# Optimization experiments

Measured on AMD Instinct MI355X. Metric: run time of the kernel, lower is better.

Reference implementation:

```python
import jax, jax.numpy as jnp
import numpy as np

EPS = 1e-6  # eps assumed for rms/unit norm (repo uses a small eps; math identical up to eps)

def rms_norm(x):
    # normalize so RMS over last dim == 1
    return x * jax.lax.rsqrt(jnp.mean(x * x, axis=-1, keepdims=True) + EPS)

def unit_norm(w):
    # normalize each output row of the weight to unit L2 norm
    return w * jax.lax.rsqrt(jnp.sum(w * w, axis=-1, keepdims=True) + EPS)

def setup_inputs() -> dict:
    key = jax.random.key(0)
    k1, k2, k3 = jax.random.split(key, 3)
    B, S, D = 4, 2048, 2048
    x = jax.random.normal(k1, (B, S, D), dtype=jnp.float32)
    w_in = jax.random.normal(k2, (3 * D, D), dtype=jnp.float32)
    w_out = jax.random.normal(k3, (D, D), dtype=jnp.float32)
    return {"x": x, "w_in": w_in, "w_out": w_out}

def reference(x, w_in, w_out):
    B, S, D = x.shape
    H = 16
    hd = D // H
    # MPLinear in-projection with unit-normalized weight rows
    qkv = jnp.einsum("bsd,fd->bsf", x, unit_norm(w_in))  # [B,S,3D]
    qkv = qkv.reshape(B, S, 3, H, hd).transpose(2, 0, 3, 1, 4)  # [3,B,H,S,hd]
    q, k, v = qkv[0], qkv[1], qkv[2]
    q = rms_norm(q)
    k = rms_norm(k)
    # scaled dot product attention, causal, default scale 1/sqrt(hd)
    scores = jnp.einsum("bhqd,bhkd->bhqk", q, k) / jnp.sqrt(jnp.float32(hd))
    causal_mask = jnp.tril(jnp.ones((S, S), dtype=bool))
    scores = jnp.where(causal_mask, scores, jnp.finfo(scores.dtype).min)
    attn = jax.nn.softmax(scores, axis=-1)
    a = jnp.einsum("bhqk,bhkd->bhqd", attn, v)  # [B,H,S,hd]
    a = rms_norm(a)
    a = a.transpose(0, 2, 1, 3).reshape(B, S, D)
    return jnp.einsum("bsd,fd->bsf", a, unit_norm(w_out))
```

## Files before the change

kernel.cpp:

```cpp
#include <hip/hip_runtime.h>

typedef float f32x4 __attribute__((ext_vector_type(4)));
typedef __bf16 bf16x8 __attribute__((ext_vector_type(8)));

#define EPSF 1e-6f
#define AS1 __attribute__((address_space(1)))
#define AS3 __attribute__((address_space(3)))

__device__ static inline void gl_lds16(const __bf16* g, __bf16* l) {
  __builtin_amdgcn_global_load_lds((const AS1 void*)g, (AS3 void*)l, 16, 0, 0);
}

__global__ __launch_bounds__(256) void prep(const float* __restrict__ x,
                                            const float* __restrict__ w_in,
                                            const float* __restrict__ w_out,
                                            __bf16* __restrict__ xb,
                                            __bf16* __restrict__ w_in_n,
                                            __bf16* __restrict__ w_out_n) {
  __shared__ float red[4];
  const int bid = blockIdx.x;
  const int t = threadIdx.x;
  if (bid < 8192) {
    const float* src = (bid < 6144) ? (w_in + (size_t)bid * 2048)
                                    : (w_out + (size_t)(bid - 6144) * 2048);
    __bf16* dst = (bid < 6144) ? (w_in_n + (size_t)bid * 2048)
                               : (w_out_n + (size_t)(bid - 6144) * 2048);
    float4 v[2];
    float ss = 0.f;
#pragma unroll
    for (int i = 0; i < 2; i++) {
      v[i] = ((const float4*)src)[t + i * 256];
      ss += v[i].x * v[i].x + v[i].y * v[i].y + v[i].z * v[i].z + v[i].w * v[i].w;
    }
#pragma unroll
    for (int m = 32; m >= 1; m >>= 1) ss += __shfl_xor(ss, m);
    if ((t & 63) == 0) red[t >> 6] = ss;
    __syncthreads();
    float tot = red[0] + red[1] + red[2] + red[3];
    float sc = rsqrtf(tot + EPSF);
#pragma unroll
    for (int i = 0; i < 2; i++) {
      int c0 = (t + i * 256) * 4;
      dst[c0 + 0] = (__bf16)(v[i].x * sc);
      dst[c0 + 1] = (__bf16)(v[i].y * sc);
      dst[c0 + 2] = (__bf16)(v[i].z * sc);
      dst[c0 + 3] = (__bf16)(v[i].w * sc);
    }
  } else {
    size_t i = ((size_t)(bid - 8192) * 256 + t) * 8;
    float4 a = ((const float4*)(x + i))[0];
    float4 b = ((const float4*)(x + i))[1];
    bf16x8 o;
    o[0] = (__bf16)a.x; o[1] = (__bf16)a.y; o[2] = (__bf16)a.z; o[3] = (__bf16)a.w;
    o[4] = (__bf16)b.x; o[5] = (__bf16)b.y; o[6] = (__bf16)b.z; o[7] = (__bf16)b.w;
    *(bf16x8*)(xb + i) = o;
  }
}

#define LDSOFF(r_, blk_) ((r_) * 64 + (((blk_) ^ ((r_) & 7)) * 8))
#define SA(bb_, c_, kt_) gl_lds16(gA + (long)(c_) * 64 * K + (long)(kt_) * 64, &As[bb_][(c_) * 4096 + t * 8])
#define SB(bb_, c_, kt_) gl_lds16(gB + (long)(c_) * 64 * K + (long)(kt_) * 64, &Bs[bb_][(c_) * 4096 + t * 8])

template <int MODE>
__global__ __launch_bounds__(512) void gemm8(const __bf16* __restrict__ A,
                                             const __bf16* __restrict__ W,
                                             float* __restrict__ C,
                                             __bf16* __restrict__ Cb,
                                             __bf16* __restrict__ Vtb,
                                             int M, int N, int K) {
  __shared__ __bf16 As[2][16384];
  __shared__ __bf16 Bs[2][16384];
  __shared__ float rsum[8][128];

  const int gx = gridDim.x;
  const int nwg = gx * gridDim.y;
  int wg = blockIdx.y * gx + blockIdx.x;
  wg = (wg & 7) * (nwg >> 3) + (wg >> 3);
  const int bx = wg % gx, by = wg / gx;

  const int t = threadIdx.x;
  const int lane = t & 63, w = t >> 6;
  const int wr = w >> 2, wc = w & 3;
  const int wrb = wr * 128, wcb = wc * 64;
  const int fr = lane & 15, fq = lane >> 4;
  const long m0 = (long)by * 256;
  const long n0 = (long)bx * 256;
  const int NT = K >> 6;

  const int srow = t >> 3;
  const int sblk = (t & 7) ^ (srow & 7);
  const __bf16* gA = A + (m0 + srow) * (long)K + sblk * 8;
  const __bf16* gB = W + (n0 + srow) * (long)K + sblk * 8;

  f32x4 acc[8][4];
#pragma unroll
  for (int i = 0; i < 8; i++)
#pragma unroll
    for (int j = 0; j < 4; j++)
#pragma unroll
      for (int c = 0; c < 4; c++) acc[i][j][c] = 0.f;

  SA(0, 0, 0); SA(0, 1, 0); SA(0, 2, 0); SA(0, 3, 0);
  SB(0, 0, 0); SB(0, 1, 0); SB(0, 2, 0); SB(0, 3, 0);
  SA(1, 0, 1); SA(1, 2, 1);
  SB(1, 0, 1); SB(1, 1, 1); SB(1, 2, 1); SB(1, 3, 1);
  asm volatile("s_waitcnt vmcnt(6)" ::: "memory");
  __builtin_amdgcn_s_barrier();

  auto tile_step = [&](int kt, int b) {
    bf16x8 a0[4][2], b01[2][2];
#pragma unroll
    for (int i = 0; i < 4; i++)
#pragma unroll
      for (int ks = 0; ks < 2; ks++)
        a0[i][ks] = *(const bf16x8*)&As[b][LDSOFF(wrb + i * 16 + fr, ks * 4 + fq)];
#pragma unroll
    for (int j = 0; j < 2; j++)
#pragma unroll
      for (int ks = 0; ks < 2; ks++)
        b01[j][ks] = *(const bf16x8*)&Bs[b][LDSOFF(wcb + j * 16 + fr, ks * 4 + fq)];
    if (kt + 1 < NT) { SA(b ^ 1, 1, kt + 1); SA(b ^ 1, 3, kt + 1); }
    __builtin_amdgcn_s_setprio(1);
#pragma unroll
    for (int i = 0; i < 4; i++)
#pragma unroll
      for (int j = 0; j < 2; j++)
#pragma unroll
        for (int ks = 0; ks < 2; ks++)
          acc[i][j] = __builtin_amdgcn_mfma_f32_16x16x32_bf16(a0[i][ks], b01[j][ks], acc[i][j], 0, 0, 0);
    __builtin_amdgcn_s_setprio(0);
    __builtin_amdgcn_sched_barrier(0);
    __builtin_amdgcn_s_barrier();

    bf16x8 b23[2][2];
#pragma unroll
    for (int j = 0; j < 2; j++)
#pragma unroll
      for (int ks = 0; ks < 2; ks++)
        b23[j][ks] = *(const bf16x8*)&Bs[b][LDSOFF(wcb + (2 + j) * 16 + fr, ks * 4 + fq)];
    if (kt + 2 < NT) { SA(b, 0, kt + 2); SA(b, 2, kt + 2); }
    __builtin_amdgcn_s_setprio(1);
#pragma unroll
    for (int i = 0; i < 4; i++)
#pragma unroll
      for (int j = 0; j < 2; j++)
#pragma unroll
        for (int ks = 0; ks < 2; ks++)
          acc[i][2 + j] = __builtin_amdgcn_mfma_f32_16x16x32_bf16(a0[i][ks], b23[j][ks], acc[i][2 + j], 0, 0, 0);
    __builtin_amdgcn_s_setprio(0);
    __builtin_amdgcn_sched_barrier(0);
    __builtin_amdgcn_s_barrier();

    bf16x8 a1[4][2];
#pragma unroll
    for (int i = 0; i < 4; i++)
#pragma unroll
      for (int ks = 0; ks < 2; ks++)
        a1[i][ks] = *(const bf16x8*)&As[b][LDSOFF(wrb + 64 + i * 16 + fr, ks * 4 + fq)];
    if (kt + 2 < NT) { SB(b, 0, kt + 2); SB(b, 1, kt + 2); SB(b, 2, kt + 2); SB(b, 3, kt + 2); }
    __builtin_amdgcn_s_setprio(1);
#pragma unroll
    for (int i = 0; i < 4; i++)
#pragma unroll
      for (int j = 0; j < 2; j++)
#pragma unroll
        for (int ks = 0; ks < 2; ks++)
          acc[4 + i][j] = __builtin_amdgcn_mfma_f32_16x16x32_bf16(a1[i][ks], b01[j][ks], acc[4 + i][j], 0, 0, 0);
#pragma unroll
    for (int i = 0; i < 4; i++)
#pragma unroll
      for (int j = 0; j < 2; j++)
#pragma unroll
        for (int ks = 0; ks < 2; ks++)
          acc[4 + i][2 + j] = __builtin_amdgcn_mfma_f32_16x16x32_bf16(a1[i][ks], b23[j][ks], acc[4 + i][2 + j], 0, 0, 0);
    __builtin_amdgcn_s_setprio(0);
    if (kt >= NT - 2)
      asm volatile("s_waitcnt vmcnt(0)" ::: "memory");
    else
      asm volatile("s_waitcnt vmcnt(6)" ::: "memory");
    __builtin_amdgcn_sched_barrier(0);
    __builtin_amdgcn_s_barrier();
  };

  for (int kt = 0; kt < NT; kt += 2) {
    tile_step(kt, 0);
    tile_step(kt + 1, 1);
  }

  if (MODE == 0) {
#pragma unroll
    for (int i = 0; i < 8; i++)
#pragma unroll
      for (int j = 0; j < 4; j++)
#pragma unroll
        for (int r = 0; r < 4; r++) {
          long row = m0 + wrb + i * 16 + fq * 4 + r;
          long col = n0 + wcb + j * 16 + fr;
          C[row * N + col] = acc[i][j][r];
        }
  } else {
    const int tt = (int)(n0 >> 11);
    const int hh = (int)(((n0 >> 7) + (wc >> 1)) & 15);
    const long e0 = (long)(wc & 1) * 64;
    if (tt < 2) {
#pragma unroll
      for (int i = 0; i < 8; i++)
#pragma unroll
        for (int r = 0; r < 4; r++) {
          float s2 = 0.f;
#pragma unroll
          for (int j = 0; j < 4; j++) s2 += acc[i][j][r] * acc[i][j][r];
          s2 += __shfl_xor(s2, 1);
          s2 += __shfl_xor(s2, 2);
          s2 += __shfl_xor(s2, 4);
          s2 += __shfl_xor(s2, 8);
          if (fr == 0) rsum[w][i * 16 + fq * 4 + r] = s2;
        }
      __syncthreads();
#pragma unroll
      for (int i = 0; i < 8; i++)
#pragma unroll
        for (int r = 0; r < 4; r++) {
          int rl = i * 16 + fq * 4 + r;
          float tot = rsum[w][rl] + rsum[w ^ 1][rl];
          float sc = rsqrtf(tot * (1.f / 128.f) + EPSF);
          long row = m0 + wrb + rl;
          long bb = row >> 11, ss = row & 2047;
          __bf16* base = Cb + ((((long)tt * 4 + bb) * 16 + hh) * 2048 + ss) * 128 + e0;
#pragma unroll
          for (int j = 0; j < 4; j++)
            base[j * 16 + fr] = (__bf16)(acc[i][j][r] * sc);
        }
    } else {
#pragma unroll
      for (int i = 0; i < 8; i++)
#pragma unroll
        for (int r = 0; r < 4; r++) {
          long row = m0 + wrb + i * 16 + fq * 4 + r;
          long bb = row >> 11, ss = row & 2047;
#pragma unroll
          for (int j = 0; j < 4; j++)
            Vtb[((bb * 16 + hh) * 128 + e0 + j * 16 + fr) * 2048 + ss] = (__bf16)acc[i][j][r];
        }
    }
  }
}

__global__ __launch_bounds__(256, 3) void attn(const __bf16* __restrict__ qkv,
                                               const __bf16* __restrict__ vt,
                                               __bf16* __restrict__ an) {
  __shared__ __bf16 Ks[64 * 128];
  __shared__ __bf16 Vs[128 * 64];
  __shared__ __bf16 plds[8][16 * 40];
  const int L = blockIdx.x;
  const int qt = L >> 6;
  const int bh = (L & 7) + 8 * ((L >> 3) & 7);
  const int t = threadIdx.x;
  const int lane = t & 63, w = t >> 6;
  const int fr = lane & 15, fq = lane >> 4;
  const int swz = fr & 7;
  const __bf16* Q = qkv + (long)bh * 262144;
  const __bf16* Kbh = qkv + 16777216L + (long)bh * 262144;
  const __bf16* Vbh = vt + (long)bh * 262144;
  const float sc2 = 0.08838834764831845f * 1.4426950408889634f;
  const float MFIX = 20.0f;
  const int b = bh >> 4, h = bh & 15;

  const __bf16* gK = Kbh + (long)(t >> 4) * 128 + ((t & 15) ^ ((t >> 4) & 7)) * 8;
  const __bf16* gV = Vbh + (long)(t >> 3) * 2048 + ((t & 7) ^ ((t >> 3) & 7)) * 8;
  __bf16* lK = &Ks[t * 8];
  __bf16* lV = &Vs[t * 8];

#pragma unroll 1
  for (int side = 0; side < 2; side++) {
    const int qi = side ? (15 - qt) : qt;
    const int q0 = qi * 128 + w * 32;
    const int cha = q0 >> 5;
    bf16x8 qf[2][4];
#pragma unroll
    for (int f = 0; f < 2; f++)
#pragma unroll
      for (int ec = 0; ec < 4; ec++)
        qf[f][ec] = *(const bf16x8*)(Q + (long)(q0 + f * 16 + fr) * 128 + ec * 32 + fq * 8);
    float lacc[2][4];
#pragma unroll
    for (int f = 0; f < 2; f++)
#pragma unroll
      for (int r = 0; r < 4; r++) lacc[f][r] = 0.f;
    f32x4 oacc[2][8];
#pragma unroll
    for (int f = 0; f < 2; f++)
#pragma unroll
      for (int e = 0; e < 8; e++)
#pragma unroll
        for (int c = 0; c < 4; c++) oacc[f][e][c] = 0.f;

    const int nst = 2 * qi + 2;
#pragma unroll 1
    for (int st = 0; st < nst; st++) {
      const long k0 = (long)st * 64;
#pragma unroll
      for (int j = 0; j < 4; j++) gl_lds16(gK + (k0 + j * 16) * 128, lK + j * 2048);
#pragma unroll
      for (int j = 0; j < 4; j++) gl_lds16(gV + (long)j * 32 * 2048 + k0, lV + j * 2048);
      __syncthreads();
#pragma unroll
      for (int half = 0; half < 2; half++) {
        const int k32 = (int)k0 + half * 32;
        const int ch = k32 >> 5;
        if (ch <= cha) {
          f32x4 sa[2][2];
#pragma unroll
          for (int f = 0; f < 2; f++)
#pragma unroll
            for (int ct = 0; ct < 2; ct++)
#pragma unroll
              for (int c = 0; c < 4; c++) sa[f][ct][c] = 0.f;
#pragma unroll
          for (int ct = 0; ct < 2; ct++) {
#pragma unroll
            for (int ec = 0; ec < 4; ec++) {
              bf16x8 kf = *(const bf16x8*)(&Ks[(half * 32 + ct * 16 + fr) * 128 +
                                               ((ec * 4 + fq) ^ swz) * 8]);
              sa[0][ct] = __builtin_amdgcn_mfma_f32_16x16x32_bf16(qf[0][ec], kf, sa[0][ct], 0, 0, 0);
              sa[1][ct] = __builtin_amdgcn_mfma_f32_16x16x32_bf16(qf[1][ec], kf, sa[1][ct], 0, 0, 0);
            }
          }
#pragma unroll
          for (int f = 0; f < 2; f++) {
            __bf16* pwf = plds[(w << 1) + f];
            if (ch == cha) {
#pragma unroll
              for (int r = 0; r < 4; r++) {
                int qg = q0 + f * 16 + fq * 4 + r;
                float p0 = exp2f(((k32 + fr) <= qg) ? sa[f][0][r] * sc2 - MFIX : -1e30f);
                float p1 = exp2f(((k32 + 16 + fr) <= qg) ? sa[f][1][r] * sc2 - MFIX : -1e30f);
                lacc[f][r] += p0 + p1;
                pwf[(fq * 4 + r) * 40 + fr] = (__bf16)p0;
                pwf[(fq * 4 + r) * 40 + 16 + fr] = (__bf16)p1;
              }
            } else {
#pragma unroll
              for (int r = 0; r < 4; r++) {
                float p0 = exp2f(__builtin_fmaf(sa[f][0][r], sc2, -MFIX));
                float p1 = exp2f(__builtin_fmaf(sa[f][1][r], sc2, -MFIX));
                lacc[f][r] += p0 + p1;
                pwf[(fq * 4 + r) * 40 + fr] = (__bf16)p0;
                pwf[(fq * 4 + r) * 40 + 16 + fr] = (__bf16)p1;
              }
            }
          }
          bf16x8 pa0 = *(const bf16x8*)(&plds[(w << 1) + 0][fr * 40 + fq * 8]);
          bf16x8 pa1 = *(const bf16x8*)(&plds[(w << 1) + 1][fr * 40 + fq * 8]);
#pragma unroll
          for (int e = 0; e < 8; e++) {
            bf16x8 vf = *(const bf16x8*)(&Vs[(e * 16 + fr) * 64 +
                                             ((half * 4 + fq) ^ swz) * 8]);
            oacc[0][e] = __builtin_amdgcn_mfma_f32_16x16x32_bf16(pa0, vf, oacc[0][e], 0, 0, 0);
            oacc[1][e] = __builtin_amdgcn_mfma_f32_16x16x32_bf16(pa1, vf, oacc[1][e], 0, 0, 0);
          }
        }
      }
      __syncthreads();
    }
#pragma unroll
    for (int f = 0; f < 2; f++)
#pragma unroll
      for (int r = 0; r < 4; r++) {
        float ls = lacc[f][r];
        ls += __shfl_xor(ls, 1);
        ls += __shfl_xor(ls, 2);
        ls += __shfl_xor(ls, 4);
        ls += __shfl_xor(ls, 8);
        float inv = 1.0f / ls;
        float ssq = 0.f;
#pragma unroll
        for (int e = 0; e < 8; e++) { float v = oacc[f][e][r] * inv; ssq += v * v; }
        ssq += __shfl_xor(ssq, 1);
        ssq += __shfl_xor(ssq, 2);
        ssq += __shfl_xor(ssq, 4);
        ssq += __shfl_xor(ssq, 8);
        float rsc = rsqrtf(ssq * (1.f / 128.f) + EPSF) * inv;
        long s = q0 + f * 16 + fq * 4 + r;
        __bf16* dst = an + ((long)b * 2048 + s) * 2048 + h * 128;
#pragma unroll
        for (int e = 0; e < 8; e++) dst[e * 16 + fr] = (__bf16)(oacc[f][e][r] * rsc);
      }
  }
}

extern "C" void kernel_launch(void* const* d_in, const int* in_sizes, int n_in,
                              void* d_out, int out_size, void* d_ws, size_t ws_size,
                              hipStream_t stream) {
  const float* x = (const float*)d_in[0];
  const float* w_in = (const float*)d_in[1];
  const float* w_out = (const float*)d_in[2];
  float* out = (float*)d_out;
  char* ws = (char*)d_ws;

  __bf16* w_in_n = (__bf16*)(ws);
  __bf16* w_out_n = (__bf16*)(ws + 25165824);
  __bf16* xb = (__bf16*)(ws + 33554432);
  __bf16* an = xb;
  __bf16* qkv = (__bf16*)(ws + 67108864);
  __bf16* vt = (__bf16*)(ws + 167772160);

  prep<<<16384, 256, 0, stream>>>(x, w_in, w_out, xb, w_in_n, w_out_n);
  gemm8<1><<<dim3(24, 32), 512, 0, stream>>>(xb, w_in_n, nullptr, qkv, vt, 8192, 6144, 2048);
  attn<<<512, 256, 0, stream>>>(qkv, vt, an);
  gemm8<0><<<dim3(8, 32), 512, 0, stream>>>(an, w_out_n, out, nullptr, nullptr, 8192, 2048, 2048);
}
```

Measured before the change: 517.9 us.

## Double-buffer K/V tiles in attention with 512-thread blocks and 256-row query tiles

The attention kernel now uses 8 waves per block covering 256 query rows, so each staged K/V tile is shared by twice as many waves. K/V tiles are double-buffered in LDS, with the next tile prefetched via global_load_lds while the current one is consumed, using vmcnt waits and raw barriers. The score-then-PV step is reorganized to process both 32-key halves of a 64-key tile together, with separate diagonal-masking paths. LDS use grows (two K/V buffers plus a larger P scratch), which lowers occupancy and halves the grid to 256 blocks, so CU load balance may suffer.

```diff
diff --git a/kernel.cpp b/kernel.cpp
--- a/kernel.cpp
+++ b/kernel.cpp
@@ -246,15 +246,15 @@
   }
 }
 
-__global__ __launch_bounds__(256, 3) void attn(const __bf16* __restrict__ qkv,
-                                               const __bf16* __restrict__ vt,
-                                               __bf16* __restrict__ an) {
-  __shared__ __bf16 Ks[64 * 128];
-  __shared__ __bf16 Vs[128 * 64];
-  __shared__ __bf16 plds[8][16 * 40];
+__global__ __launch_bounds__(512) void attn(const __bf16* __restrict__ qkv,
+                                            const __bf16* __restrict__ vt,
+                                            __bf16* __restrict__ an) {
+  __shared__ __bf16 Ks[2][64 * 128];
+  __shared__ __bf16 Vs[2][128 * 64];
+  __shared__ __bf16 plds[32][16 * 40];
   const int L = blockIdx.x;
-  const int qt = L >> 6;
-  const int bh = (L & 7) + 8 * ((L >> 3) & 7);
+  const int qp = L >> 6;
+  const int bh = L & 63;
   const int t = threadIdx.x;
   const int lane = t & 63, w = t >> 6;
   const int fr = lane & 15, fq = lane >> 4;
@@ -268,14 +268,24 @@
 
   const __bf16* gK = Kbh + (long)(t >> 4) * 128 + ((t & 15) ^ ((t >> 4) & 7)) * 8;
   const __bf16* gV = Vbh + (long)(t >> 3) * 2048 + ((t & 7) ^ ((t >> 3) & 7)) * 8;
-  __bf16* lK = &Ks[t * 8];
-  __bf16* lV = &Vs[t * 8];
+
+  auto stage = [&](int st, int buf) {
+    const long k0 = (long)st * 64;
+    gl_lds16(gK + k0 * 128, &Ks[buf][t * 8]);
+    gl_lds16(gK + (k0 + 32) * 128, &Ks[buf][4096 + t * 8]);
+    gl_lds16(gV + k0, &Vs[buf][t * 8]);
+    gl_lds16(gV + 64L * 2048 + k0, &Vs[buf][4096 + t * 8]);
+  };
 
 #pragma unroll 1
   for (int side = 0; side < 2; side++) {
-    const int qi = side ? (15 - qt) : qt;
-    const int q0 = qi * 128 + w * 32;
+    const int qi = side ? (7 - qp) : qp;
+    const int q0 = qi * 256 + w * 32;
     const int cha = q0 >> 5;
+    const int nst = 4 * qi + 4;
+
+    stage(0, 0);
+    stage(1, 1);
     bf16x8 qf[2][4];
 #pragma unroll
     for (int f = 0; f < 2; f++)
@@ -295,73 +305,132 @@
 #pragma unroll
         for (int c = 0; c < 4; c++) oacc[f][e][c] = 0.f;
 
-    const int nst = 2 * qi + 2;
 #pragma unroll 1
     for (int st = 0; st < nst; st++) {
-      const long k0 = (long)st * 64;
-#pragma unroll
-      for (int j = 0; j < 4; j++) gl_lds16(gK + (k0 + j * 16) * 128, lK + j * 2048);
-#pragma unroll
-      for (int j = 0; j < 4; j++) gl_lds16(gV + (long)j * 32 * 2048 + k0, lV + j * 2048);
-      __syncthreads();
-#pragma unroll
-      for (int half = 0; half < 2; half++) {
-        const int k32 = (int)k0 + half * 32;
-        const int ch = k32 >> 5;
-        if (ch <= cha) {
-          f32x4 sa[2][2];
+      if (st + 1 < nst)
+        asm volatile("s_waitcnt vmcnt(4)" ::: "memory");
+      else
+        asm volatile("s_waitcnt vmcnt(0)" ::: "memory");
+      __builtin_amdgcn_s_barrier();
+      const __bf16* Kb = Ks[st & 1];
+      const __bf16* Vb = Vs[st & 1];
+      const int k0 = st * 64;
+      const int ch0 = 2 * st, ch1 = 2 * st + 1;
+      if (ch1 <= cha) {
+        f32x4 sa[2][2][2];
+#pragma unroll
+        for (int hh2 = 0; hh2 < 2; hh2++)
 #pragma unroll
           for (int f = 0; f < 2; f++)
 #pragma unroll
             for (int ct = 0; ct < 2; ct++)
 #pragma unroll
-              for (int c = 0; c < 4; c++) sa[f][ct][c] = 0.f;
-#pragma unroll
-          for (int ct = 0; ct < 2; ct++) {
+              for (int c = 0; c < 4; c++) sa[hh2][f][ct][c] = 0.f;
+#pragma unroll
+        for (int hh2 = 0; hh2 < 2; hh2++)
+#pragma unroll
+          for (int ct = 0; ct < 2; ct++)
 #pragma unroll
             for (int ec = 0; ec < 4; ec++) {
-              bf16x8 kf = *(const bf16x8*)(&Ks[(half * 32 + ct * 16 + fr) * 128 +
+              bf16x8 kf = *(const bf16x8*)(&Kb[(hh2 * 32 + ct * 16 + fr) * 128 +
                                                ((ec * 4 + fq) ^ swz) * 8]);
-              sa[0][ct] = __builtin_amdgcn_mfma_f32_16x16x32_bf16(qf[0][ec], kf, sa[0][ct], 0, 0, 0);
-              sa[1][ct] = __builtin_amdgcn_mfma_f32_16x16x32_bf16(qf[1][ec], kf, sa[1][ct], 0, 0, 0);
+              sa[hh2][0][ct] = __builtin_amdgcn_mfma_f32_16x16x32_bf16(qf[0][ec], kf, sa[hh2][0][ct], 0, 0, 0);
+              sa[hh2][1][ct] = __builtin_amdgcn_mfma_f32_16x16x32_bf16(qf[1][ec], kf, sa[hh2][1][ct], 0, 0, 0);
             }
-          }
+#pragma unroll
+        for (int f = 0; f < 2; f++) {
+          __bf16* pwf = plds[((w << 1) + f) * 2 + 0];
+#pragma unroll
+          for (int r = 0; r < 4; r++) {
+            float p0 = exp2f(__builtin_fmaf(sa[0][f][0][r], sc2, -MFIX));
+            float p1 = exp2f(__builtin_fmaf(sa[0][f][1][r], sc2, -MFIX));
+            lacc[f][r] += p0 + p1;
+            pwf[(fq * 4 + r) * 40 + fr] = (__bf16)p0;
+            pwf[(fq * 4 + r) * 40 + 16 + fr] = (__bf16)p1;
+          }
+        }
+        if (ch1 == cha) {
+          const int k32 = k0 + 32;
 #pragma unroll
           for (int f = 0; f < 2; f++) {
-            __bf16* pwf = plds[(w << 1) + f];
-            if (ch == cha) {
-#pragma unroll
-              for (int r = 0; r < 4; r++) {
-                int qg = q0 + f * 16 + fq * 4 + r;
-                float p0 = exp2f(((k32 + fr) <= qg) ? sa[f][0][r] * sc2 - MFIX : -1e30f);
-                float p1 = exp2f(((k32 + 16 + fr) <= qg) ? sa[f][1][r] * sc2 - MFIX : -1e30f);
-                lacc[f][r] += p0 + p1;
-                pwf[(fq * 4 + r) * 40 + fr] = (__bf16)p0;
-                pwf[(fq * 4 + r) * 40 + 16 + fr] = (__bf16)p1;
-              }
-            } else {
-#pragma unroll
-              for (int r = 0; r < 4; r++) {
-                float p0 = exp2f(__builtin_fmaf(sa[f][0][r], sc2, -MFIX));
-                float p1 = exp2f(__builtin_fmaf(sa[f][1][r], sc2, -MFIX));
-                lacc[f][r] += p0 + p1;
-                pwf[(fq * 4 + r) * 40 + fr] = (__bf16)p0;
-                pwf[(fq * 4 + r) * 40 + 16 + fr] = (__bf16)p1;
-              }
+            __bf16* pwf = plds[((w << 1) + f) * 2 + 1];
+#pragma unroll
+            for (int r = 0; r < 4; r++) {
+              int qg = q0 + f * 16 + fq * 4 + r;
+              float p0 = exp2f(((k32 + fr) <= qg) ? sa[1][f][0][r] * sc2 - MFIX : -1e30f);
+              float p1 = exp2f(((k32 + 16 + fr) <= qg) ? sa[1][f][1][r] * sc2 - MFIX : -1e30f);
+              lacc[f][r] += p0 + p1;
+              pwf[(fq * 4 + r) * 40 + fr] = (__bf16)p0;
+              pwf[(fq * 4 + r) * 40 + 16 + fr] = (__bf16)p1;
             }
           }
-          bf16x8 pa0 = *(const bf16x8*)(&plds[(w << 1) + 0][fr * 40 + fq * 8]);
-          bf16x8 pa1 = *(const bf16x8*)(&plds[(w << 1) + 1][fr * 40 + fq * 8]);
+        } else {
+#pragma unroll
+          for (int f = 0; f < 2; f++) {
+            __bf16* pwf = plds[((w << 1) + f) * 2 + 1];
+#pragma unroll
+            for (int r = 0; r < 4; r++) {
+              float p0 = exp2f(__builtin_fmaf(sa[1][f][0][r], sc2, -MFIX));
+              float p1 = exp2f(__builtin_fmaf(sa[1][f][1][r], sc2, -MFIX));
+              lacc[f][r] += p0 + p1;
+              pwf[(fq * 4 + r) * 40 + fr] = (__bf16)p0;
+              pwf[(fq * 4 + r) * 40 + 16 + fr] = (__bf16)p1;
+            }
+          }
+        }
+#pragma unroll
+        for (int hh2 = 0; hh2 < 2; hh2++) {
+          bf16x8 pa0 = *(const bf16x8*)(&plds[((w << 1) + 0) * 2 + hh2][fr * 40 + fq * 8]);
+          bf16x8 pa1 = *(const bf16x8*)(&plds[((w << 1) + 1) * 2 + hh2][fr * 40 + fq * 8]);
 #pragma unroll
           for (int e = 0; e < 8; e++) {
-            bf16x8 vf = *(const bf16x8*)(&Vs[(e * 16 + fr) * 64 +
-                                             ((half * 4 + fq) ^ swz) * 8]);
+            bf16x8 vf = *(const bf16x8*)(&Vb[(e * 16 + fr) * 64 +
+                                             ((hh2 * 4 + fq) ^ swz) * 8]);
             oacc[0][e] = __builtin_amdgcn_mfma_f32_16x16x32_bf16(pa0, vf, oacc[0][e], 0, 0, 0);
             oacc[1][e] = __builtin_amdgcn_mfma_f32_16x16x32_bf16(pa1, vf, oacc[1][e], 0, 0, 0);
           }
         }
+      } else if (ch0 <= cha) {
+        f32x4 sa[2][2];
+#pragma unroll
+        for (int f = 0; f < 2; f++)
+#pragma unroll
+          for (int ct = 0; ct < 2; ct++)
+#pragma unroll
+            for (int c = 0; c < 4; c++) sa[f][ct][c] = 0.f;
+#pragma unroll
+        for (int ct = 0; ct < 2; ct++)
+#pragma unroll
+          for (int ec = 0; ec < 4; ec++) {
+            bf16x8 kf = *(const bf16x8*)(&Kb[(ct * 16 + fr) * 128 +
+                                             ((ec * 4 + fq) ^ swz) * 8]);
+            sa[0][ct] = __builtin_amdgcn_mfma_f32_16x16x32_bf16(qf[0][ec], kf, sa[0][ct], 0, 0, 0);
+            sa[1][ct] = __builtin_amdgcn_mfma_f32_16x16x32_bf16(qf[1][ec], kf, sa[1][ct], 0, 0, 0);
+          }
+#pragma unroll
+        for (int f = 0; f < 2; f++) {
+          __bf16* pwf = plds[((w << 1) + f) * 2 + 0];
+#pragma unroll
+          for (int r = 0; r < 4; r++) {
+            int qg = q0 + f * 16 + fq * 4 + r;
+            float p0 = exp2f(((k0 + fr) <= qg) ? sa[f][0][r] * sc2 - MFIX : -1e30f);
+            float p1 = exp2f(((k0 + 16 + fr) <= qg) ? sa[f][1][r] * sc2 - MFIX : -1e30f);
+            lacc[f][r] += p0 + p1;
+            pwf[(fq * 4 + r) * 40 + fr] = (__bf16)p0;
+            pwf[(fq * 4 + r) * 40 + 16 + fr] = (__bf16)p1;
+          }
+        }
+        bf16x8 pa0 = *(const bf16x8*)(&plds[((w << 1) + 0) * 2 + 0][fr * 40 + fq * 8]);
+        bf16x8 pa1 = *(const bf16x8*)(&plds[((w << 1) + 1) * 2 + 0][fr * 40 + fq * 8]);
+#pragma unroll
+        for (int e = 0; e < 8; e++) {
+          bf16x8 vf = *(const bf16x8*)(&Vb[(e * 16 + fr) * 64 + (fq ^ swz) * 8]);
+          oacc[0][e] = __builtin_amdgcn_mfma_f32_16x16x32_bf16(pa0, vf, oacc[0][e], 0, 0, 0);
+          oacc[1][e] = __builtin_amdgcn_mfma_f32_16x16x32_bf16(pa1, vf, oacc[1][e], 0, 0, 0);
+        }
       }
-      __syncthreads();
+      __builtin_amdgcn_s_barrier();
+      if (st + 2 < nst) stage(st + 2, st & 1);
     }
 #pragma unroll
     for (int f = 0; f < 2; f++)
@@ -407,6 +476,6 @@
 
   prep<<<16384, 256, 0, stream>>>(x, w_in, w_out, xb, w_in_n, w_out_n);
   gemm8<1><<<dim3(24, 32), 512, 0, stream>>>(xb, w_in_n, nullptr, qkv, vt, 8192, 6144, 2048);
-  attn<<<512, 256, 0, stream>>>(qkv, vt, an);
+  attn<<<256, 512, 0, stream>>>(qkv, vt, an);
   gemm8<0><<<dim3(8, 32), 512, 0, stream>>>(an, w_out_n, out, nullptr, nullptr, 8192, 2048, 2048);
 }
```

Measured after the change: 519.6 us. Within noise of the previous version (+0.3%).

## Drop shared-memory K/V staging in attention, have each wave read K/V directly

Applied to the files above, without the earlier changes.

The attention kernel no longer stages K and V tiles through LDS with block-wide barriers. Each wave now owns its own 32-row query chunk, and the four waves of a block take chunks spaced 16 apart to balance the causal work. Each wave loads K and V fragments straight from global memory per 32-key chunk, and the grid doubles to 1024 blocks. This removes __syncthreads and LDS traffic and allows more concurrency. The cost is that K/V reuse across waves is lost, so global/L2 traffic rises and load latency is no longer hidden by an explicit prefetch.

```diff
diff --git a/kernel.cpp b/kernel.cpp
--- a/kernel.cpp
+++ b/kernel.cpp
@@ -246,19 +246,16 @@
   }
 }
 
-__global__ __launch_bounds__(256, 3) void attn(const __bf16* __restrict__ qkv,
-                                               const __bf16* __restrict__ vt,
-                                               __bf16* __restrict__ an) {
-  __shared__ __bf16 Ks[64 * 128];
-  __shared__ __bf16 Vs[128 * 64];
+__global__ __launch_bounds__(256) void attn(const __bf16* __restrict__ qkv,
+                                            const __bf16* __restrict__ vt,
+                                            __bf16* __restrict__ an) {
   __shared__ __bf16 plds[8][16 * 40];
   const int L = blockIdx.x;
-  const int qt = L >> 6;
-  const int bh = (L & 7) + 8 * ((L >> 3) & 7);
+  const int qb = L >> 6;
+  const int bh = L & 63;
   const int t = threadIdx.x;
   const int lane = t & 63, w = t >> 6;
   const int fr = lane & 15, fq = lane >> 4;
-  const int swz = fr & 7;
   const __bf16* Q = qkv + (long)bh * 262144;
   const __bf16* Kbh = qkv + 16777216L + (long)bh * 262144;
   const __bf16* Vbh = vt + (long)bh * 262144;
@@ -266,127 +263,113 @@
   const float MFIX = 20.0f;
   const int b = bh >> 4, h = bh & 15;
 
-  const __bf16* gK = Kbh + (long)(t >> 4) * 128 + ((t & 15) ^ ((t >> 4) & 7)) * 8;
-  const __bf16* gV = Vbh + (long)(t >> 3) * 2048 + ((t & 7) ^ ((t >> 3) & 7)) * 8;
-  __bf16* lK = &Ks[t * 8];
-  __bf16* lV = &Vs[t * 8];
+  const int cha = qb + 16 * w;
+  const int q0 = cha * 32;
+
+  bf16x8 qf[2][4];
+#pragma unroll
+  for (int f = 0; f < 2; f++)
+#pragma unroll
+    for (int ec = 0; ec < 4; ec++)
+      qf[f][ec] = *(const bf16x8*)(Q + (long)(q0 + f * 16 + fr) * 128 + ec * 32 + fq * 8);
+  float lacc[2][4];
+#pragma unroll
+  for (int f = 0; f < 2; f++)
+#pragma unroll
+    for (int r = 0; r < 4; r++) lacc[f][r] = 0.f;
+  f32x4 oacc[2][8];
+#pragma unroll
+  for (int f = 0; f < 2; f++)
+#pragma unroll
+    for (int e = 0; e < 8; e++)
+#pragma unroll
+      for (int c = 0; c < 4; c++) oacc[f][e][c] = 0.f;
 
 #pragma unroll 1
-  for (int side = 0; side < 2; side++) {
-    const int qi = side ? (15 - qt) : qt;
-    const int q0 = qi * 128 + w * 32;
-    const int cha = q0 >> 5;
-    bf16x8 qf[2][4];
+  for (int ch = 0; ch <= cha; ch++) {
+    const int k32 = ch * 32;
+    bf16x8 vf[8];
+#pragma unroll
+    for (int e = 0; e < 8; e++)
+      vf[e] = *(const bf16x8*)(Vbh + (long)(e * 16 + fr) * 2048 + k32 + fq * 8);
+    f32x4 sa[2][2];
 #pragma unroll
     for (int f = 0; f < 2; f++)
 #pragma unroll
+      for (int ct = 0; ct < 2; ct++)
+#pragma unroll
+        for (int c = 0; c < 4; c++) sa[f][ct][c] = 0.f;
+#pragma unroll
+    for (int ct = 0; ct < 2; ct++) {
+      bf16x8 kf[4];
+#pragma unroll
       for (int ec = 0; ec < 4; ec++)
-        qf[f][ec] = *(const bf16x8*)(Q + (long)(q0 + f * 16 + fr) * 128 + ec * 32 + fq * 8);
-    float lacc[2][4];
-#pragma unroll
-    for (int f = 0; f < 2; f++)
-#pragma unroll
-      for (int r = 0; r < 4; r++) lacc[f][r] = 0.f;
-    f32x4 oacc[2][8];
-#pragma unroll
-    for (int f = 0; f < 2; f++)
-#pragma unroll
-      for (int e = 0; e < 8; e++)
-#pragma unroll
-        for (int c = 0; c < 4; c++) oacc[f][e][c] = 0.f;
-
-    const int nst = 2 * qi + 2;
-#pragma unroll 1
-    for (int st = 0; st < nst; st++) {
-      const long k0 = (long)st * 64;
-#pragma unroll
-      for (int j = 0; j < 4; j++) gl_lds16(gK + (k0 + j * 16) * 128, lK + j * 2048);
-#pragma unroll
-      for (int j = 0; j < 4; j++) gl_lds16(gV + (long)j * 32 * 2048 + k0, lV + j * 2048);
-      __syncthreads();
-#pragma unroll
-      for (int half = 0; half < 2; half++) {
-        const int k32 = (int)k0 + half * 32;
-        const int ch = k32 >> 5;
-        if (ch <= cha) {
-          f32x4 sa[2][2];
-#pragma unroll
-          for (int f = 0; f < 2; f++)
-#pragma unroll
-            for (int ct = 0; ct < 2; ct++)
-#pragma unroll
-              for (int c = 0; c < 4; c++) sa[f][ct][c] = 0.f;
-#pragma unroll
-          for (int ct = 0; ct < 2; ct++) {
-#pragma unroll
-            for (int ec = 0; ec < 4; ec++) {
-              bf16x8 kf = *(const bf16x8*)(&Ks[(half * 32 + ct * 16 + fr) * 128 +
-                                               ((ec * 4 + fq) ^ swz) * 8]);
-              sa[0][ct] = __builtin_amdgcn_mfma_f32_16x16x32_bf16(qf[0][ec], kf, sa[0][ct], 0, 0, 0);
-              sa[1][ct] = __builtin_amdgcn_mfma_f32_16x16x32_bf16(qf[1][ec], kf, sa[1][ct], 0, 0, 0);
-            }
-          }
-#pragma unroll
-          for (int f = 0; f < 2; f++) {
-            __bf16* pwf = plds[(w << 1) + f];
-            if (ch == cha) {
-#pragma unroll
-              for (int r = 0; r < 4; r++) {
-                int qg = q0 + f * 16 + fq * 4 + r;
-                float p0 = exp2f(((k32 + fr) <= qg) ? sa[f][0][r] * sc2 - MFIX : -1e30f);
-                float p1 = exp2f(((k32 + 16 + fr) <= qg) ? sa[f][1][r] * sc2 - MFIX : -1e30f);
-                lacc[f][r] += p0 + p1;
-                pwf[(fq * 4 + r) * 40 + fr] = (__bf16)p0;
-                pwf[(fq * 4 + r) * 40 + 16 + fr] = (__bf16)p1;
-              }
-            } else {
-#pragma unroll
-              for (int r = 0; r < 4; r++) {
-                float p0 = exp2f(__builtin_fmaf(sa[f][0][r], sc2, -MFIX));
-                float p1 = exp2f(__builtin_fmaf(sa[f][1][r], sc2, -MFIX));
-                lacc[f][r] += p0 + p1;
-                pwf[(fq * 4 + r) * 40 + fr] = (__bf16)p0;
-                pwf[(fq * 4 + r) * 40 + 16 + fr] = (__bf16)p1;
-              }
-            }
-          }
-          bf16x8 pa0 = *(const bf16x8*)(&plds[(w << 1) + 0][fr * 40 + fq * 8]);
-          bf16x8 pa1 = *(const bf16x8*)(&plds[(w << 1) + 1][fr * 40 + fq * 8]);
-#pragma unroll
-          for (int e = 0; e < 8; e++) {
-            bf16x8 vf = *(const bf16x8*)(&Vs[(e * 16 + fr) * 64 +
-                                             ((half * 4 + fq) ^ swz) * 8]);
-            oacc[0][e] = __builtin_amdgcn_mfma_f32_16x16x32_bf16(pa0, vf, oacc[0][e], 0, 0, 0);
-            oacc[1][e] = __builtin_amdgcn_mfma_f32_16x16x32_bf16(pa1, vf, oacc[1][e], 0, 0, 0);
-          }
-        }
+        kf[ec] = *(const bf16x8*)(Kbh + (long)(k32 + ct * 16 + fr) * 128 + ec * 32 + fq * 8);
+#pragma unroll
+      for (int ec = 0; ec < 4; ec++) {
+        sa[0][ct] = __builtin_amdgcn_mfma_f32_16x16x32_bf16(qf[0][ec], kf[ec], sa[0][ct], 0, 0, 0);
+        sa[1][ct] = __builtin_amdgcn_mfma_f32_16x16x32_bf16(qf[1][ec], kf[ec], sa[1][ct], 0, 0, 0);
       }
-      __syncthreads();
-    }
-#pragma unroll
-    for (int f = 0; f < 2; f++)
-#pragma unroll
-      for (int r = 0; r < 4; r++) {
-        float ls = lacc[f][r];
-        ls += __shfl_xor(ls, 1);
-        ls += __shfl_xor(ls, 2);
-        ls += __shfl_xor(ls, 4);
-        ls += __shfl_xor(ls, 8);
-        float inv = 1.0f / ls;
-        float ssq = 0.f;
-#pragma unroll
-        for (int e = 0; e < 8; e++) { float v = oacc[f][e][r] * inv; ssq += v * v; }
-        ssq += __shfl_xor(ssq, 1);
-        ssq += __shfl_xor(ssq, 2);
-        ssq += __shfl_xor(ssq, 4);
-        ssq += __shfl_xor(ssq, 8);
-        float rsc = rsqrtf(ssq * (1.f / 128.f) + EPSF) * inv;
-        long s = q0 + f * 16 + fq * 4 + r;
-        __bf16* dst = an + ((long)b * 2048 + s) * 2048 + h * 128;
-#pragma unroll
-        for (int e = 0; e < 8; e++) dst[e * 16 + fr] = (__bf16)(oacc[f][e][r] * rsc);
+    }
+    if (ch == cha) {
+#pragma unroll
+      for (int f = 0; f < 2; f++) {
+        __bf16* pwf = plds[(w << 1) + f];
+#pragma unroll
+        for (int r = 0; r < 4; r++) {
+          int qg = q0 + f * 16 + fq * 4 + r;
+          float p0 = exp2f(((k32 + fr) <= qg) ? sa[f][0][r] * sc2 - MFIX : -1e30f);
+          float p1 = exp2f(((k32 + 16 + fr) <= qg) ? sa[f][1][r] * sc2 - MFIX : -1e30f);
+          lacc[f][r] += p0 + p1;
+          pwf[(fq * 4 + r) * 40 + fr] = (__bf16)p0;
+          pwf[(fq * 4 + r) * 40 + 16 + fr] = (__bf16)p1;
+        }
       }
+    } else {
+#pragma unroll
+      for (int f = 0; f < 2; f++) {
+        __bf16* pwf = plds[(w << 1) + f];
+#pragma unroll
+        for (int r = 0; r < 4; r++) {
+          float p0 = exp2f(__builtin_fmaf(sa[f][0][r], sc2, -MFIX));
+          float p1 = exp2f(__builtin_fmaf(sa[f][1][r], sc2, -MFIX));
+          lacc[f][r] += p0 + p1;
+          pwf[(fq * 4 + r) * 40 + fr] = (__bf16)p0;
+          pwf[(fq * 4 + r) * 40 + 16 + fr] = (__bf16)p1;
+        }
+      }
+    }
+    bf16x8 pa0 = *(const bf16x8*)(&plds[(w << 1) + 0][fr * 40 + fq * 8]);
+    bf16x8 pa1 = *(const bf16x8*)(&plds[(w << 1) + 1][fr * 40 + fq * 8]);
+#pragma unroll
+    for (int e = 0; e < 8; e++) {
+      oacc[0][e] = __builtin_amdgcn_mfma_f32_16x16x32_bf16(pa0, vf[e], oacc[0][e], 0, 0, 0);
+      oacc[1][e] = __builtin_amdgcn_mfma_f32_16x16x32_bf16(pa1, vf[e], oacc[1][e], 0, 0, 0);
+    }
   }
+#pragma unroll
+  for (int f = 0; f < 2; f++)
+#pragma unroll
+    for (int r = 0; r < 4; r++) {
+      float ls = lacc[f][r];
+      ls += __shfl_xor(ls, 1);
+      ls += __shfl_xor(ls, 2);
+      ls += __shfl_xor(ls, 4);
+      ls += __shfl_xor(ls, 8);
+      float inv = 1.0f / ls;
+      float ssq = 0.f;
+#pragma unroll
+      for (int e = 0; e < 8; e++) { float v = oacc[f][e][r] * inv; ssq += v * v; }
+      ssq += __shfl_xor(ssq, 1);
+      ssq += __shfl_xor(ssq, 2);
+      ssq += __shfl_xor(ssq, 4);
+      ssq += __shfl_xor(ssq, 8);
+      float rsc = rsqrtf(ssq * (1.f / 128.f) + EPSF) * inv;
+      long s = q0 + f * 16 + fq * 4 + r;
+      __bf16* dst = an + ((long)b * 2048 + s) * 2048 + h * 128;
+#pragma unroll
+      for (int e = 0; e < 8; e++) dst[e * 16 + fr] = (__bf16)(oacc[f][e][r] * rsc);
+    }
 }
 
 extern "C" void kernel_launch(void* const* d_in, const int* in_sizes, int n_in,
@@ -407,6 +390,6 @@
 
   prep<<<16384, 256, 0, stream>>>(x, w_in, w_out, xb, w_in_n, w_out_n);
   gemm8<1><<<dim3(24, 32), 512, 0, stream>>>(xb, w_in_n, nullptr, qkv, vt, 8192, 6144, 2048);
-  attn<<<512, 256, 0, stream>>>(qkv, vt, an);
+  attn<<<1024, 256, 0, stream>>>(qkv, vt, an);
   gemm8<0><<<dim3(8, 32), 512, 0, stream>>>(an, w_out_n, out, nullptr, nullptr, 8192, 2048, 2048);
 }
```

New measurement: 662.0 us. 1.28x slower.
